# Kernel optimization log

Hardware: AMD Instinct MI355X
Metric: run time of the kernel (lower is better)

The kernel has to match this reference:

```python
import jax, jax.numpy as jnp
import numpy as np

N, C = 8192, 64

def setup_inputs() -> dict:
    key = jax.random.key(0)
    k1, k2, k3 = jax.random.split(key, 3)
    values = jax.random.normal(k1, (N, C), dtype=jnp.float32)
    coords = jax.random.uniform(k2, (N, 2), dtype=jnp.float32)
    spacing = jax.random.uniform(k3, (2,), dtype=jnp.float32)
    shift = jnp.zeros((2,), dtype=jnp.float32)
    return {"values": values, "coords": coords, "spacing": spacing, "shift": shift}


def reference(values, coords, spacing, shift):
    # grid_mode branch of upsample_nn: 3 shifted copies of the coord grid
    x, y = coords[:, 0], coords[:, 1]
    new_coords = jnp.concatenate([
        jnp.stack((x + spacing[0], y + spacing[1]), axis=1),
        jnp.stack((x, y + spacing[1]), axis=1),
        jnp.stack((x + spacing[0], y), axis=1),
    ], axis=0)  # [3N, 2]

    # Diffs = ||(new_coords - shift)[:,None] - coords[None,:]||, argmin over coords.
    # argmin of the L2 norm == argmin of the squared distance, so use the
    # expanded form to avoid materializing the [3N, N, 2] difference tensor.
    a = new_coords - shift  # [3N, 2]
    d2 = (jnp.sum(a * a, axis=1)[:, None]
          + jnp.sum(coords * coords, axis=1)[None, :]
          - 2.0 * a @ coords.T)  # [3N, N]
    idx = jnp.argmin(d2, axis=1)  # [3N]
    new_values = values[idx]      # [3N, C]

    out_values = jnp.concatenate([values, new_values], axis=0)   # [4N, C]
    out_coords = jnp.concatenate([coords, new_coords], axis=0)   # [4N, 2]
    return out_values, out_coords
```

## Files before the change

kernel.cpp:

```cpp
#include <hip/hip_runtime.h>

#pragma clang fp contract(off)

#define N_PTS 8192
#define C_DIM 64
#define NQ (3 * N_PTS)
#define G 64
#define NCELL (G * G)
#define MARGIN 1.2e-5f
#define HCELL (1.0f / 64.0f)
#define QBLOCKS (NQ / 32)
#define CBLOCKS 256


__device__ __forceinline__ unsigned int fsortkey(float f) {
    const unsigned int u = __float_as_uint(f);
    return (u & 0x80000000u) ? ~u : (u | 0x80000000u);
}
__device__ __forceinline__ float finvkey(unsigned int e) {
    const unsigned int u = (e & 0x80000000u) ? (e & 0x7fffffffu) : ~e;
    return __uint_as_float(u);
}

__device__ __forceinline__ void shift_query(int g, float x, float y,
                                            float sx, float sy,
                                            float& nx, float& ny) {
    if (g == 0)      { nx = x + sx; ny = y + sy; }
    else if (g == 1) { nx = x;      ny = y + sy; }
    else             { nx = x + sx; ny = y; }
}

__global__ __launch_bounds__(1024) void build_kernel(
    const float2* __restrict__ coords2,
    float4* __restrict__ sorted,
    int* __restrict__ starts)
{
#pragma clang fp contract(off)
    __shared__ unsigned int lhist[NCELL];
    __shared__ unsigned int wsum[16];
    const int t    = threadIdx.x;
    const int lane = t & 63;
    const int w    = t >> 6;

    #pragma unroll
    for (int k = 0; k < 4; ++k) lhist[4 * t + k] = 0u;
    __syncthreads();

    #pragma unroll
    for (int k = 0; k < 8; ++k) {
        const int i = t + 1024 * k;
        const float2 c = coords2[i];
        int cx = (int)(c.x * 64.0f); cx = min(max(cx, 0), G - 1);
        int cy = (int)(c.y * 64.0f); cy = min(max(cy, 0), G - 1);
        atomicAdd(&lhist[cy * G + cx], 1u);
    }
    __syncthreads();

    const unsigned h0 = lhist[4 * t + 0], h1 = lhist[4 * t + 1];
    const unsigned h2 = lhist[4 * t + 2], h3 = lhist[4 * t + 3];
    const unsigned tot = h0 + h1 + h2 + h3;

    unsigned v = tot;
    #pragma unroll
    for (int s = 1; s < 64; s <<= 1) {
        const unsigned o = __shfl_up(v, s, 64);
        if (lane >= s) v += o;
    }
    if (lane == 63) wsum[w] = v;
    __syncthreads();
    if (t < 16) {
        unsigned x = wsum[t];
        #pragma unroll
        for (int s = 1; s < 16; s <<= 1) {
            const unsigned o = __shfl_up(x, s, 16);
            if ((t & 15) >= s) x += o;
        }
        wsum[t] = x;
    }
    __syncthreads();
    const unsigned woff = (w == 0) ? 0u : wsum[w - 1];
    const unsigned e0 = v + woff - tot;
    const unsigned e1 = e0 + h0, e2 = e1 + h1, e3 = e2 + h2;
    starts[4 * t + 0] = (int)e0; starts[4 * t + 1] = (int)e1;
    starts[4 * t + 2] = (int)e2; starts[4 * t + 3] = (int)e3;
    lhist[4 * t + 0] = e0; lhist[4 * t + 1] = e1;
    lhist[4 * t + 2] = e2; lhist[4 * t + 3] = e3;
    if (t == 0) starts[NCELL] = N_PTS;
    __syncthreads();

    #pragma unroll
    for (int k = 0; k < 8; ++k) {
        const int i = t + 1024 * k;
        const float2 c = coords2[i];
        int cx = (int)(c.x * 64.0f); cx = min(max(cx, 0), G - 1);
        int cy = (int)(c.y * 64.0f); cy = min(max(cy, 0), G - 1);
        const unsigned pos = atomicAdd(&lhist[cy * G + cx], 1u);
        const float p0 = c.x * c.x;
        const float p1 = c.y * c.y;
        const float sc = p0 + p1;
        sorted[pos] = make_float4(c.x, c.y, sc, __int_as_float(i));
    }
}

__global__ __launch_bounds__(256) void mega_kernel(
    const float4* __restrict__ sorted,
    const int* __restrict__ starts,
    const float4* __restrict__ values4,
    const float2* __restrict__ coords2,
    const float* __restrict__ spacing,
    const float* __restrict__ shift,
    float4* __restrict__ out_values4,
    float2* __restrict__ out_coords)
{
#pragma clang fp contract(off)
    if (blockIdx.x >= QBLOCKS) {
        const int blk = blockIdx.x - QBLOCKS;
        const int c4  = threadIdx.x & 15;
        #pragma unroll
        for (int it = 0; it < 2; ++it) {
            const int row = blk * 32 + it * 16 + (threadIdx.x >> 4);
            out_values4[row * 16 + c4] = values4[row * 16 + c4];
            if (c4 == 0) out_coords[row] = coords2[row];
        }
        return;
    }

    const int lane = threadIdx.x & 7;
    const int q    = blockIdx.x * 32 + (threadIdx.x >> 3);
    const int g    = q >> 13;
    const int k    = q & (N_PTS - 1);

    const float4 me = sorted[k];
    const int b = __float_as_int(me.w);

    float nx, ny;
    shift_query(g, me.x, me.y, spacing[0], spacing[1], nx, ny);
    const float ax = nx - shift[0];
    const float ay = ny - shift[1];
    const float sa = (ax * ax) + (ay * ay);

    int cx = (int)floorf(ax * 64.0f); cx = min(max(cx, 0), G - 1);
    int cy = (int)floorf(ay * 64.0f); cy = min(max(cy, 0), G - 1);
    const float dxo = fmaxf(fmaxf(ax - 1.0f, -ax), 0.0f);
    const float dyo = fmaxf(fmaxf(ay - 1.0f, -ay), 0.0f);
    (void)dyo;

    float best = INFINITY;
    int   bi   = 0x7fffffff;

#define EVAL_SPAN(S, E)                                                     \
    for (int i = (S) + lane; i < (E); i += 8) {                             \
        const float4 pt = sorted[i];                                        \
        const float p   = ax * pt.x;                                        \
        const float dv  = __builtin_fmaf(ay, pt.y, p);                      \
        const float t1  = sa + pt.z;                                        \
        const float d2  = t1 - (2.0f * dv);                                 \
        const int   j   = __float_as_int(pt.w);                             \
        if (d2 < best || (d2 == best && j < bi)) { best = d2; bi = j; }     \
    }

    const int xa = max(cx - 1, 0), xb = min(cx + 1, G - 1);
    const int ya = max(cy - 1, 0), yb = min(cy + 1, G - 1);
    for (int yy = ya; yy <= yb; ++yy) {
        const int s = starts[yy * G + xa];
        const int e = starts[yy * G + xb + 1];
        EVAL_SPAN(s, e)
    }

    unsigned long long key =
        ((unsigned long long)fsortkey(best) << 32) | (unsigned int)bi;
    #pragma unroll
    for (int m = 1; m < 8; m <<= 1) {
        const unsigned long long o = __shfl_xor(key, m, 8);
        if (o < key) key = o;
    }
    best = finvkey((unsigned int)(key >> 32));
    bi   = (int)(unsigned int)key;

    const float U = best + MARGIN;

    float sr = sqrtf(fmaxf(U - dxo * dxo, 0.0f));
    sr = fminf(sr, 4.0f);
    const int ylo = max((int)floorf((ay - sr) * 64.0f), 0);
    const int yhi = min((int)floorf((ay + sr) * 64.0f), G - 1);

    float sc_ = fminf(sqrtf(U), 4.0f);
    const int xlo_c = max((int)floorf((ax - sc_) * 64.0f), 0);
    const int xhi_c = min((int)floorf((ax + sc_) * 64.0f), G - 1);

    const bool skip = (ylo >= ya) && (yhi <= yb) && (xlo_c >= xa) && (xhi_c <= xb);

    if (!skip) {
        for (int yy = ylo; yy <= yhi; ++yy) {
            const float ry0 = (float)yy * HCELL;
            const float ry1 = ry0 + HCELL;
            const float vy  = fmaxf(fmaxf(ay - ry1, ry0 - ay), 0.0f);
            const float r2  = U - vy * vy;
            if (r2 < 0.0f) continue;
            float s = fminf(sqrtf(r2), 4.0f);
            const int xl = max((int)floorf((ax - s) * 64.0f), 0);
            const int xh = min((int)floorf((ax + s) * 64.0f), G - 1);
            const int ss = starts[yy * G + xl];
            const int ee = starts[yy * G + xh + 1];
            EVAL_SPAN(ss, ee)
        }
        key = ((unsigned long long)fsortkey(best) << 32) | (unsigned int)bi;
        #pragma unroll
        for (int m = 1; m < 8; m <<= 1) {
            const unsigned long long o = __shfl_xor(key, m, 8);
            if (o < key) key = o;
        }
        bi = (int)(unsigned int)key;
    }
#undef EVAL_SPAN

    const int qi  = g * N_PTS + b;
    const int row = N_PTS + qi;
    out_values4[row * 16 + 2 * lane + 0] = values4[bi * 16 + 2 * lane + 0];
    out_values4[row * 16 + 2 * lane + 1] = values4[bi * 16 + 2 * lane + 1];
    if (lane == 0) out_coords[row] = make_float2(nx, ny);
}

extern "C" void kernel_launch(void* const* d_in, const int* in_sizes, int n_in,
                              void* d_out, int out_size, void* d_ws, size_t ws_size,
                              hipStream_t stream)
{
    const float* values  = (const float*)d_in[0];
    const float* coords  = (const float*)d_in[1];
    const float* spacing = (const float*)d_in[2];
    const float* shift   = (const float*)d_in[3];

    float* out_values = (float*)d_out;
    float2* out_coords = (float2*)(out_values + (size_t)4 * N_PTS * C_DIM);

    char* ws = (char*)d_ws;
    float4* sorted = (float4*)ws;
    int* starts    = (int*)(ws + 131072);

    build_kernel<<<1, 1024, 0, stream>>>((const float2*)coords, sorted, starts);

    mega_kernel<<<QBLOCKS + CBLOCKS, 256, 0, stream>>>(
        sorted, starts, (const float4*)values, (const float2*)coords,
        spacing, shift, (float4*)out_values, out_coords);
}
```

Measured before the change: 26.97 us.

## Overlap passthrough copy with grid build and batch cell-range loads in queries

New measurement: 24.59 us. 8.8% less time.

```diff
diff --git a/kernel.cpp b/kernel.cpp
--- a/kernel.cpp
+++ b/kernel.cpp
@@ -10,7 +10,7 @@
 #define MARGIN 1.2e-5f
 #define HCELL (1.0f / 64.0f)
 #define QBLOCKS (NQ / 32)
-#define CBLOCKS 256
+#define COPYBLKS 128
 
 
 __device__ __forceinline__ unsigned int fsortkey(float f) {
@@ -30,12 +30,24 @@
     else             { nx = x + sx; ny = y; }
 }
 
-__global__ __launch_bounds__(1024) void build_kernel(
+__global__ __launch_bounds__(1024) void build_copy_kernel(
     const float2* __restrict__ coords2,
+    const float4* __restrict__ values4,
     float4* __restrict__ sorted,
-    int* __restrict__ starts)
+    int* __restrict__ starts,
+    float4* __restrict__ out_values4,
+    float2* __restrict__ out_coords)
 {
 #pragma clang fp contract(off)
+    if (blockIdx.x > 0) {
+        const int t   = threadIdx.x;
+        const int row = ((int)blockIdx.x - 1) * 64 + (t >> 4);
+        const int c4  = t & 15;
+        out_values4[row * 16 + c4] = values4[row * 16 + c4];
+        if (c4 == 0) out_coords[row] = coords2[row];
+        return;
+    }
+
     __shared__ unsigned int lhist[NCELL];
     __shared__ unsigned int wsum[16];
     const int t    = threadIdx.x;
@@ -46,13 +58,17 @@
     for (int k = 0; k < 4; ++k) lhist[4 * t + k] = 0u;
     __syncthreads();
 
+    float2 cpt[8];
+    int    cell[8];
     #pragma unroll
     for (int k = 0; k < 8; ++k) {
         const int i = t + 1024 * k;
         const float2 c = coords2[i];
+        cpt[k] = c;
         int cx = (int)(c.x * 64.0f); cx = min(max(cx, 0), G - 1);
         int cy = (int)(c.y * 64.0f); cy = min(max(cy, 0), G - 1);
-        atomicAdd(&lhist[cy * G + cx], 1u);
+        cell[k] = cy * G + cx;
+        atomicAdd(&lhist[cell[k]], 1u);
     }
     __syncthreads();
 
@@ -91,10 +107,8 @@
     #pragma unroll
     for (int k = 0; k < 8; ++k) {
         const int i = t + 1024 * k;
-        const float2 c = coords2[i];
-        int cx = (int)(c.x * 64.0f); cx = min(max(cx, 0), G - 1);
-        int cy = (int)(c.y * 64.0f); cy = min(max(cy, 0), G - 1);
-        const unsigned pos = atomicAdd(&lhist[cy * G + cx], 1u);
+        const float2 c = cpt[k];
+        const unsigned pos = atomicAdd(&lhist[cell[k]], 1u);
         const float p0 = c.x * c.x;
         const float p1 = c.y * c.y;
         const float sc = p0 + p1;
@@ -102,29 +116,16 @@
     }
 }
 
-__global__ __launch_bounds__(256) void mega_kernel(
+__global__ __launch_bounds__(256) void query_kernel(
     const float4* __restrict__ sorted,
     const int* __restrict__ starts,
     const float4* __restrict__ values4,
-    const float2* __restrict__ coords2,
     const float* __restrict__ spacing,
     const float* __restrict__ shift,
     float4* __restrict__ out_values4,
     float2* __restrict__ out_coords)
 {
 #pragma clang fp contract(off)
-    if (blockIdx.x >= QBLOCKS) {
-        const int blk = blockIdx.x - QBLOCKS;
-        const int c4  = threadIdx.x & 15;
-        #pragma unroll
-        for (int it = 0; it < 2; ++it) {
-            const int row = blk * 32 + it * 16 + (threadIdx.x >> 4);
-            out_values4[row * 16 + c4] = values4[row * 16 + c4];
-            if (c4 == 0) out_coords[row] = coords2[row];
-        }
-        return;
-    }
-
     const int lane = threadIdx.x & 7;
     const int q    = blockIdx.x * 32 + (threadIdx.x >> 3);
     const int g    = q >> 13;
@@ -142,8 +143,6 @@
     int cx = (int)floorf(ax * 64.0f); cx = min(max(cx, 0), G - 1);
     int cy = (int)floorf(ay * 64.0f); cy = min(max(cy, 0), G - 1);
     const float dxo = fmaxf(fmaxf(ax - 1.0f, -ax), 0.0f);
-    const float dyo = fmaxf(fmaxf(ay - 1.0f, -ay), 0.0f);
-    (void)dyo;
 
     float best = INFINITY;
     int   bi   = 0x7fffffff;
@@ -161,10 +160,17 @@
 
     const int xa = max(cx - 1, 0), xb = min(cx + 1, G - 1);
     const int ya = max(cy - 1, 0), yb = min(cy + 1, G - 1);
-    for (int yy = ya; yy <= yb; ++yy) {
-        const int s = starts[yy * G + xa];
-        const int e = starts[yy * G + xb + 1];
-        EVAL_SPAN(s, e)
+    int ss1[3], ee1[3];
+    #pragma unroll
+    for (int r = 0; r < 3; ++r) {
+        const int yy = ya + r;
+        const bool vv = (yy <= yb);
+        ss1[r] = vv ? starts[yy * G + xa] : 0;
+        ee1[r] = vv ? starts[yy * G + xb + 1] : 0;
+    }
+    #pragma unroll
+    for (int r = 0; r < 3; ++r) {
+        EVAL_SPAN(ss1[r], ee1[r])
     }
 
     unsigned long long key =
@@ -184,25 +190,35 @@
     const int ylo = max((int)floorf((ay - sr) * 64.0f), 0);
     const int yhi = min((int)floorf((ay + sr) * 64.0f), G - 1);
 
-    float sc_ = fminf(sqrtf(U), 4.0f);
-    const int xlo_c = max((int)floorf((ax - sc_) * 64.0f), 0);
-    const int xhi_c = min((int)floorf((ax + sc_) * 64.0f), G - 1);
+    float scw = fminf(sqrtf(U), 4.0f);
+    const int xlo_c = max((int)floorf((ax - scw) * 64.0f), 0);
+    const int xhi_c = min((int)floorf((ax + scw) * 64.0f), G - 1);
 
     const bool skip = (ylo >= ya) && (yhi <= yb) && (xlo_c >= xa) && (xhi_c <= xb);
 
     if (!skip) {
-        for (int yy = ylo; yy <= yhi; ++yy) {
-            const float ry0 = (float)yy * HCELL;
-            const float ry1 = ry0 + HCELL;
-            const float vy  = fmaxf(fmaxf(ay - ry1, ry0 - ay), 0.0f);
-            const float r2  = U - vy * vy;
-            if (r2 < 0.0f) continue;
-            float s = fminf(sqrtf(r2), 4.0f);
-            const int xl = max((int)floorf((ax - s) * 64.0f), 0);
-            const int xh = min((int)floorf((ax + s) * 64.0f), G - 1);
-            const int ss = starts[yy * G + xl];
-            const int ee = starts[yy * G + xh + 1];
-            EVAL_SPAN(ss, ee)
+        for (int yy0 = ylo; yy0 <= yhi; yy0 += 4) {
+            int ss2[4], ee2[4];
+            #pragma unroll
+            for (int r = 0; r < 4; ++r) {
+                const int yy = yy0 + r;
+                bool vv = (yy <= yhi);
+                const float ry0 = (float)yy * HCELL;
+                const float vy  = fmaxf(fmaxf(ay - ry0 - HCELL, ry0 - ay), 0.0f);
+                const float r2  = U - vy * vy;
+                vv = vv && (r2 >= 0.0f);
+                const float s = fminf(sqrtf(fmaxf(r2, 0.0f)), 4.0f);
+                int xl = max((int)floorf((ax - s) * 64.0f), 0);
+                int xh = min((int)floorf((ax + s) * 64.0f), G - 1);
+                vv = vv && (xl <= xh);
+                vv = vv && !(yy >= ya && yy <= yb && xl >= xa && xh <= xb);
+                ss2[r] = vv ? starts[yy * G + xl] : 0;
+                ee2[r] = vv ? starts[yy * G + xh + 1] : 0;
+            }
+            #pragma unroll
+            for (int r = 0; r < 4; ++r) {
+                EVAL_SPAN(ss2[r], ee2[r])
+            }
         }
         key = ((unsigned long long)fsortkey(best) << 32) | (unsigned int)bi;
         #pragma unroll
@@ -237,9 +253,11 @@
     float4* sorted = (float4*)ws;
     int* starts    = (int*)(ws + 131072);
 
-    build_kernel<<<1, 1024, 0, stream>>>((const float2*)coords, sorted, starts);
-
-    mega_kernel<<<QBLOCKS + CBLOCKS, 256, 0, stream>>>(
-        sorted, starts, (const float4*)values, (const float2*)coords,
-        spacing, shift, (float4*)out_values, out_coords);
-}
+    build_copy_kernel<<<1 + COPYBLKS, 1024, 0, stream>>>(
+        (const float2*)coords, (const float4*)values,
+        sorted, starts, (float4*)out_values, out_coords);
+
+    query_kernel<<<QBLOCKS, 256, 0, stream>>>(
+        sorted, starts, (const float4*)values, spacing, shift,
+        (float4*)out_values, out_coords);
+}
```
